# Kernel tuning notes

Measured on AMD Instinct MI355X. Metric: run time of the kernel, lower is better.

## Reference

```python
import jax, jax.numpy as jnp
import numpy as np

T, B, I, H, L = 512, 32, 1024, 1024, 2


def setup_inputs() -> dict:
    key = jax.random.key(0)
    ks = jax.random.split(key, 10)
    stdv = 1.0 / np.sqrt(H)
    u = lambda k, shape: jax.random.uniform(k, shape, jnp.float32, -stdv, stdv)
    return {
        "x": jax.random.normal(ks[0], (T, B, I), jnp.float32),
        "h0": jnp.zeros((L, B, H), jnp.float32),
        "c0": jnp.zeros((L, B, H), jnp.float32),
        "W0": u(ks[1], (4 * H, I)),
        "R0": u(ks[2], (4 * H, H)),
        "bi0": u(ks[3], (4 * H,)),
        "bh0": u(ks[4], (4 * H,)),
        "W1": u(ks[5], (4 * H, H)),
        "R1": u(ks[6], (4 * H, H)),
        "bi1": u(ks[7], (4 * H,)),
        "bh1": u(ks[8], (4 * H,)),
    }


def _run_layer(x, h_init, c_init, W, R, bi, bh):
    # Precompute input projection for all timesteps: [T, B, 4H]
    xg = jnp.einsum('tbi,gi->tbg', x, W) + bi

    def step(carry, xg_t):
        h, c = carry
        gates = jax.nn.sigmoid(xg_t + h @ R.T + bh)  # [B, 4H]
        i_g, o_g, z_g, f_g = jnp.split(gates, 4, axis=-1)
        c = c * f_g + z_g - i_g          # subtractive cell update
        h = jax.nn.sigmoid(c) - o_g      # subtractive output
        return (h, c), h

    (hT, cT), out = jax.lax.scan(step, (h_init, c_init), xg)
    return out, hT, cT


def reference(x, h0, c0, W0, R0, bi0, bh0, W1, R1, bi1, bh1):
    layers = [(W0, R0, bi0, bh0), (W1, R1, bi1, bh1)]
    out = x
    h_finals, c_finals = [], []
    for l, (W, R, bi, bh) in enumerate(layers):
        out, hT, cT = _run_layer(out, h0[l], c0[l], W, R, bi, bh)
        h_finals.append(hT)
        c_finals.append(cT)
    return out, (jnp.stack(h_finals), jnp.stack(c_finals))
```

## Files before the change

kernel.cpp:

```cpp
#include <hip/hip_runtime.h>

typedef unsigned short ushort_t;
typedef unsigned int uint_t;
typedef __bf16 bf16x8 __attribute__((ext_vector_type(8)));
typedef float f32x4 __attribute__((ext_vector_type(4)));

#define T_STEPS 512
#define NWG 256

union bfu { uint4 u; bf16x8 v; };

__device__ __forceinline__ float bf2f(ushort_t u) {
  union { unsigned u; float f; } v; v.u = ((unsigned)u) << 16; return v.f;
}
__device__ __forceinline__ ushort_t f2bf(float f) {
  union { float f; unsigned u; } v; v.f = f;
  unsigned r = (v.u + 0x7FFFu + ((v.u >> 16) & 1u)) >> 16;
  return (ushort_t)r;
}
__device__ __forceinline__ uint_t pack2(float a, float b) {
  return (uint_t)f2bf(a) | ((uint_t)f2bf(b) << 16);
}
__device__ __forceinline__ float sigf(float x) {
  return 1.0f / (1.0f + __expf(-x));
}

__global__ void __launch_bounds__(256) cvt_f32_bf16(
    const float* __restrict__ in, ushort_t* __restrict__ outp, int n4) {
  int i = blockIdx.x * 256 + threadIdx.x;
  const int stride = gridDim.x * 256;
  for (; i < n4; i += stride) {
    float4 v = ((const float4*)in)[i];
    ushort4 o;
    o.x = f2bf(v.x); o.y = f2bf(v.y); o.z = f2bf(v.z); o.w = f2bf(v.w);
    ((ushort4*)outp)[i] = o;
  }
}

__global__ void __launch_bounds__(256) init_h(
    const float* __restrict__ h0_all, ushort_t* __restrict__ hpp0,
    ushort_t* __restrict__ hpp1) {
  int i = blockIdx.x * 256 + threadIdx.x;
  int l = i >> 13, j = i & 8191;
  float4 v = ((const float4*)(h0_all + l * 32768))[j];
  ushort4 o;
  o.x = f2bf(v.x); o.y = f2bf(v.y); o.z = f2bf(v.z); o.w = f2bf(v.w);
  ((ushort4*)(l ? (hpp1 + 32768) : (hpp0 + 98304)))[j] = o;
}

__global__ void __launch_bounds__(256, 1) gemm_xg(
    const float* __restrict__ X, const ushort_t* __restrict__ Wm,
    const float* __restrict__ bi, ushort_t* __restrict__ outp) {
  __shared__ char smem[65536];
  const int tid = threadIdx.x;
  const int lane = tid & 63, w = tid >> 6;
  const int m0 = blockIdx.x * 128, n0 = blockIdx.y * 128;
  const int wr = w >> 1, wc = w & 1;
  const int lr = lane & 15, kg = lane >> 4;
  const int ar_ = tid & 127;
  const int abq = (tid >> 7) * 4;

  f32x4 acc[4][4] = {};
  float4 fa[8];

  auto stageA_issue = [&](int kt) {
    const float* src = X + (size_t)(m0 + ar_) * 1024 + kt * 64 + abq * 8;
#pragma unroll
    for (int i = 0; i < 4; ++i) {
      fa[2 * i] = *(const float4*)(src + i * 8);
      fa[2 * i + 1] = *(const float4*)(src + i * 8 + 4);
    }
  };
  auto stageA_write = [&](int p) {
    char* sA = smem + p * 32768;
#pragma unroll
    for (int i = 0; i < 4; ++i) {
      int blk = abq + i;
      uint4 o;
      o.x = pack2(fa[2 * i].x, fa[2 * i].y);
      o.y = pack2(fa[2 * i].z, fa[2 * i].w);
      o.z = pack2(fa[2 * i + 1].x, fa[2 * i + 1].y);
      o.w = pack2(fa[2 * i + 1].z, fa[2 * i + 1].w);
      *(uint4*)(sA + ar_ * 128 + ((blk ^ (ar_ & 7)) << 4)) = o;
    }
  };
  auto stageB = [&](int kt, int p) {
    const int ks = kt * 64;
    char* sB = smem + p * 32768 + 16384;
#pragma unroll
    for (int i = 0; i < 4; ++i) {
      int wi = w * 4 + i;
      int e = wi * 64 + lane;
      int row = e >> 3, pb = e & 7;
      int kb = pb ^ (row & 7);
      const ushort_t* gB = Wm + (size_t)(n0 + row) * 1024 + ks + kb * 8;
      __builtin_amdgcn_global_load_lds(
          (const __attribute__((address_space(1))) void*)gB,
          (__attribute__((address_space(3))) void*)(sB + wi * 1024), 16, 0, 0);
    }
  };

  stageA_issue(0);
  stageB(0, 0);
  stageA_write(0);
  __syncthreads();
#pragma unroll 1
  for (int kt = 0; kt < 16; ++kt) {
    const int p = kt & 1;
    if (kt < 15) { stageA_issue(kt + 1); stageB(kt + 1, p ^ 1); }
    const char* sA = smem + p * 32768;
    const char* sB = sA + 16384;
#pragma unroll
    for (int k2 = 0; k2 < 2; ++k2) {
      bf16x8 af[4], bf[4];
#pragma unroll
      for (int mt = 0; mt < 4; ++mt) {
        int ar = wr * 64 + mt * 16 + lr;
        int kb = k2 * 4 + kg;
        af[mt] = *(const bf16x8*)(sA + ar * 128 + ((kb ^ (ar & 7)) << 4));
      }
#pragma unroll
      for (int nt = 0; nt < 4; ++nt) {
        int br = wc * 64 + nt * 16 + lr;
        int kb = k2 * 4 + kg;
        bf[nt] = *(const bf16x8*)(sB + br * 128 + ((kb ^ (br & 7)) << 4));
      }
#pragma unroll
      for (int mt = 0; mt < 4; ++mt)
#pragma unroll
        for (int nt = 0; nt < 4; ++nt)
          acc[mt][nt] = __builtin_amdgcn_mfma_f32_16x16x32_bf16(
              af[mt], bf[nt], acc[mt][nt], 0, 0, 0);
    }
    if (kt < 15) stageA_write(p ^ 1);
    __syncthreads();
  }
#pragma unroll
  for (int nt = 0; nt < 4; ++nt) {
    int gc = n0 + wc * 64 + nt * 16 + lr;
    int pc = ((gc & 1023) >> 3) * 32 + (gc & 7) * 4 + (gc >> 10);
    float bv = bi[gc];
#pragma unroll
    for (int mt = 0; mt < 4; ++mt) {
#pragma unroll
      for (int r = 0; r < 4; ++r) {
        int gr = m0 + wr * 64 + mt * 16 + kg * 4 + r;
        outp[(size_t)gr * 4096 + pc] = f2bf(acc[mt][nt][r] + bv);
      }
    }
  }
}

#define GLD4(dst, addr)                                        \
  asm volatile("global_load_dwordx4 %0, %1, off sc0 sc1"      \
               : "=v"(dst) : "v"(addr))
#define WAITN(N)                                               \
  do {                                                         \
    asm volatile("s_waitcnt vmcnt(" #N ")" ::: "memory");      \
    __builtin_amdgcn_sched_barrier(0);                         \
  } while (0)

__global__ void __launch_bounds__(512, 1) fused_rec(
    const ushort_t* __restrict__ xg0p, const float* __restrict__ R0,
    const float* __restrict__ R1, const float* __restrict__ W1,
    const float* __restrict__ bh0, const float* __restrict__ bi1,
    const float* __restrict__ bh1, const float* __restrict__ c0_all,
    float* __restrict__ out_f, float* __restrict__ hfinb,
    float* __restrict__ cfinb, ushort_t* __restrict__ hpp0,
    ushort_t* __restrict__ hpp1, uint_t* __restrict__ flags0,
    uint_t* __restrict__ flags1) {
  extern __shared__ char smem[];
  char* hl = smem;
  float* gl = (float*)(smem + 131072);

  const int tid = threadIdx.x;
  const int wg = blockIdx.x;
  const int layer = wg >> 7;
  const int wgl = wg & 127;
  const int j0 = wgl * 8;
  const int lane = tid & 63, w = tid >> 6;
  const int n16 = (w & 1) << 4;
  const int kq = w >> 1;
  const int lr16 = lane & 15, kg = lane >> 4;
  const int b = (tid >> 3) & 31, jj = tid & 7;
  const int rx = lr16 & 7;

  uint_t* fown = layer ? flags1 : flags0;
  uint_t* foth = layer ? flags0 : flags1;

  const int c = n16 + lr16;
  const int r_w = ((c >> 3) << 10) + j0 + (c & 7);
  bf16x8 breg[16];
  if (layer == 0) {
#pragma unroll
    for (int i = 0; i < 8; ++i) {
      const float* src = R0 + (size_t)r_w * 1024 + kq * 256 + i * 32 + kg * 8;
      float4 f0 = *(const float4*)src;
      float4 f1 = *(const float4*)(src + 4);
      bfu o;
      o.u.x = pack2(f0.x, f0.y); o.u.y = pack2(f0.z, f0.w);
      o.u.z = pack2(f1.x, f1.y); o.u.w = pack2(f1.z, f1.w);
      breg[i] = o.v;
    }
  } else {
#pragma unroll
    for (int i = 0; i < 16; ++i) {
      int k = kq * 512 + i * 32 + kg * 8;
      const float* src = (k < 1024) ? (R1 + (size_t)r_w * 1024 + k)
                                    : (W1 + (size_t)r_w * 1024 + (k - 1024));
      float4 f0 = *(const float4*)src;
      float4 f1 = *(const float4*)(src + 4);
      bfu o;
      o.u.x = pack2(f0.x, f0.y); o.u.y = pack2(f0.z, f0.w);
      o.u.z = pack2(f1.x, f1.y); o.u.w = pack2(f1.z, f1.w);
      breg[i] = o.v;
    }
  }

  float bhv[4];
#pragma unroll
  for (int g = 0; g < 4; ++g) {
    int gi = g * 1024 + j0 + jj;
    bhv[g] = layer ? (bi1[gi] + bh1[gi]) : bh0[gi];
  }
  const int cidx = b * 1024 + j0 + jj;
  float c_st = c0_all[layer * 32768 + cidx];
  uint_t* hppd = (uint_t*)(layer ? hpp1 : hpp0);

  const char* xgbase = (const char*)xg0p +
      ((size_t)b * 4096 + (size_t)wgl * 32 + (size_t)jj * 4) * 2;
  uint2 xgu = {0, 0}, xgn = {0, 0};
  if (layer == 0)
    asm volatile("global_load_dwordx2 %0, %1, off" : "=v"(xgu) : "v"(xgbase));
  __syncthreads();

#pragma unroll 1
  for (int t = 0; t < T_STEPS; ++t) {
    {
      const int genOwn = t;
      const int genOth = layer ? (t + 1) : (t - 3);
      if (tid < 128) {
        while ((int)__hip_atomic_load(&fown[tid], __ATOMIC_RELAXED,
                                      __HIP_MEMORY_SCOPE_AGENT) < genOwn)
          __builtin_amdgcn_s_sleep(1);
      } else if (tid < 256) {
        while ((int)__hip_atomic_load(&foth[tid - 128], __ATOMIC_RELAXED,
                                      __HIP_MEMORY_SCOPE_AGENT) < genOth)
          __builtin_amdgcn_s_sleep(1);
      }
      __syncthreads();
      asm volatile("" ::: "memory");
    }

    uint4 hv[16];
    if (layer == 0) {
      if (t + 1 < T_STEPS)
        asm volatile("global_load_dwordx2 %0, %1, off"
                     : "=v"(xgn) : "v"(xgbase + (size_t)(t + 1) * 262144));
      const char* hsrc =
          (const char*)hpp0 + (((t + 3) & 3) << 16) + tid * 16;
#pragma unroll
      for (int l = 0; l < 8; ++l) GLD4(hv[l], hsrc + l * 8192);
      WAITN(0);
#pragma unroll
      for (int l = 0; l < 8; ++l) {
        int idx = l * 512 + tid;
        int row = idx >> 7, kb = idx & 127;
        *(uint4*)(hl + row * 2048 + ((kb ^ (row & 7)) << 4)) = hv[l];
      }
    } else {
      const char* h1src =
          (const char*)hpp1 + (((t + 1) & 1) << 16) + tid * 16;
      const char* h0src =
          (const char*)hpp0 + ((t & 3) << 16) + tid * 16;
#pragma unroll
      for (int l = 0; l < 8; ++l) GLD4(hv[l], h1src + l * 8192);
#pragma unroll
      for (int l = 0; l < 8; ++l) GLD4(hv[8 + l], h0src + l * 8192);
      WAITN(8);
#pragma unroll
      for (int l = 0; l < 8; ++l) {
        int idx = l * 512 + tid;
        int row = idx >> 7, kb = idx & 127;
        *(uint4*)(hl + row * 2048 + ((kb ^ (row & 7)) << 4)) = hv[l];
      }
      WAITN(0);
#pragma unroll
      for (int l = 0; l < 8; ++l) {
        int idx = l * 512 + tid;
        int row = idx >> 7, kb = idx & 127;
        *(uint4*)(hl + 65536 + row * 2048 + ((kb ^ (row & 7)) << 4)) =
            hv[8 + l];
      }
    }
    __syncthreads();

    f32x4 acc0 = {0.f, 0.f, 0.f, 0.f}, acc1 = {0.f, 0.f, 0.f, 0.f};
    if (layer == 0) {
      const char* a0 = hl + lr16 * 2048;
      const char* a1 = hl + (16 + lr16) * 2048;
#pragma unroll
      for (int i = 0; i < 8; ++i) {
        int kb = kq * 32 + i * 4 + kg;
        bf16x8 av0 = *(const bf16x8*)(a0 + ((kb ^ rx) << 4));
        bf16x8 av1 = *(const bf16x8*)(a1 + ((kb ^ rx) << 4));
        acc0 = __builtin_amdgcn_mfma_f32_16x16x32_bf16(av0, breg[i], acc0,
                                                       0, 0, 0);
        acc1 = __builtin_amdgcn_mfma_f32_16x16x32_bf16(av1, breg[i], acc1,
                                                       0, 0, 0);
      }
    } else {
      const char* buf = hl + ((kq >> 1) ? 65536 : 0);
      const char* a0 = buf + lr16 * 2048;
      const char* a1 = buf + (16 + lr16) * 2048;
#pragma unroll
      for (int i = 0; i < 16; ++i) {
        int kb = (kq & 1) * 64 + i * 4 + kg;
        bf16x8 av0 = *(const bf16x8*)(a0 + ((kb ^ rx) << 4));
        bf16x8 av1 = *(const bf16x8*)(a1 + ((kb ^ rx) << 4));
        acc0 = __builtin_amdgcn_mfma_f32_16x16x32_bf16(av0, breg[i], acc0,
                                                       0, 0, 0);
        acc1 = __builtin_amdgcn_mfma_f32_16x16x32_bf16(av1, breg[i], acc1,
                                                       0, 0, 0);
      }
    }
#pragma unroll
    for (int r = 0; r < 4; ++r) {
      gl[(kq * 32 + kg * 4 + r) * 33 + n16 + lr16] = acc0[r];
      gl[(kq * 32 + 16 + kg * 4 + r) * 33 + n16 + lr16] = acc1[r];
    }
    __syncthreads();

    if (tid < 256) {
      float pre[4];
#pragma unroll
      for (int g = 0; g < 4; ++g) {
        int col = g * 8 + jj;
        pre[g] = gl[(0 * 32 + b) * 33 + col] + gl[(1 * 32 + b) * 33 + col] +
                 gl[(2 * 32 + b) * 33 + col] + gl[(3 * 32 + b) * 33 + col] +
                 bhv[g];
      }
      if (layer == 0) {
        pre[0] += bf2f((ushort_t)(xgu.x & 0xffff));
        pre[1] += bf2f((ushort_t)(xgu.x >> 16));
        pre[2] += bf2f((ushort_t)(xgu.y & 0xffff));
        pre[3] += bf2f((ushort_t)(xgu.y >> 16));
      }
      float ig = sigf(pre[0]), og = sigf(pre[1]);
      float zg = sigf(pre[2]), fg = sigf(pre[3]);
      c_st = c_st * fg + zg - ig;
      float hv_ = sigf(c_st) - og;
      if (layer) out_f[(size_t)t * 32768 + cidx] = hv_;

      ushort_t hb = f2bf(hv_);
      int partner = __shfl_down((int)hb, 1, 64);
      if ((tid & 1) == 0) {
        uint_t packed =
            (uint_t)hb | (((uint_t)(unsigned short)partner) << 16);
        uint_t* dst = hppd +
            ((layer ? ((t & 1) << 14) : ((t & 3) << 14)) + (cidx >> 1));
        asm volatile("global_store_dword %0, %1, off sc0 sc1"
                     :: "v"(dst), "v"(packed) : "memory");
      }
      if (t == T_STEPS - 1) {
        hfinb[layer * 32768 + cidx] = hv_;
        cfinb[layer * 32768 + cidx] = c_st;
      }
    }

    asm volatile("s_waitcnt vmcnt(0)" ::: "memory");
    __syncthreads();
    if (tid == 0)
      __hip_atomic_store(&fown[wgl], (uint_t)(t + 1), __ATOMIC_RELAXED,
                         __HIP_MEMORY_SCOPE_AGENT);
    if (layer == 0) xgu = xgn;
  }
}

extern "C" void kernel_launch(void* const* d_in, const int* in_sizes, int n_in,
                              void* d_out, int out_size, void* d_ws,
                              size_t ws_size, hipStream_t stream) {
  (void)in_sizes; (void)n_in; (void)out_size; (void)ws_size;
  const float* x = (const float*)d_in[0];
  const float* h0 = (const float*)d_in[1];
  const float* c0 = (const float*)d_in[2];
  const float* W0 = (const float*)d_in[3];
  const float* R0 = (const float*)d_in[4];
  const float* bi0 = (const float*)d_in[5];
  const float* bh0 = (const float*)d_in[6];
  const float* W1 = (const float*)d_in[7];
  const float* R1 = (const float*)d_in[8];
  const float* bi1 = (const float*)d_in[9];
  const float* bh1 = (const float*)d_in[10];
  float* outp = (float*)d_out;

  char* ws = (char*)d_ws;
  ushort_t* Wbf0 = (ushort_t*)ws;
  ushort_t* xg0p = (ushort_t*)(ws + 8388608);
  ushort_t* hpp0 = (ushort_t*)(ws + 8388608 + 134217728);
  ushort_t* hpp1 = (ushort_t*)((char*)hpp0 + 262144);
  uint_t* flags0 = (uint_t*)((char*)hpp1 + 131072);
  uint_t* flags1 = flags0 + 128;

  const int REC_LDS = 131072 + 4 * 32 * 33 * 4;
  (void)hipFuncSetAttribute((const void*)fused_rec,
                            hipFuncAttributeMaxDynamicSharedMemorySize,
                            REC_LDS);
  (void)hipMemsetAsync(flags0, 0, 256 * sizeof(uint_t), stream);

  float* hfinb = outp + 16777216;
  float* cfinb = hfinb + 65536;

  cvt_f32_bf16<<<dim3(1024), dim3(256), 0, stream>>>(W0, Wbf0, 1048576);
  init_h<<<dim3(64), dim3(256), 0, stream>>>(h0, hpp0, hpp1);
  gemm_xg<<<dim3(128, 32), dim3(256), 0, stream>>>(x, Wbf0, bi0, xg0p);
  fused_rec<<<dim3(NWG), dim3(512), REC_LDS, stream>>>(
      xg0p, R0, R1, W1, bh0, bi1, bh1, c0, outp, hfinb, cfinb,
      hpp0, hpp1, flags0, flags1);
}
```

Baseline: 4.425 ms.

## Prefetch layer-0 h one step ahead in layer 1 and split its GEMM

Layer-1 workgroups now compute the input-projection half (W1 times layer-0 h) from an h0 tile loaded in the previous step. They run it while the recurrent h1 tile is still in flight, then do the R1 half once h1 arrives. This needs layer 1 to wait for layer 0 to be two steps ahead instead of one. The xg prefetch register is dropped in favour of issuing the next load at the end of the step, and the partial-sum LDS layout is changed to a padded row-of-132 layout. The aim is to hide global-load latency on the serial critical path, at the cost of tighter cross-layer coupling and more registers.

```diff
diff --git a/kernel.cpp b/kernel.cpp
--- a/kernel.cpp
+++ b/kernel.cpp
@@ -204,10 +204,8 @@
     }
   } else {
 #pragma unroll
-    for (int i = 0; i < 16; ++i) {
-      int k = kq * 512 + i * 32 + kg * 8;
-      const float* src = (k < 1024) ? (R1 + (size_t)r_w * 1024 + k)
-                                    : (W1 + (size_t)r_w * 1024 + (k - 1024));
+    for (int i = 0; i < 8; ++i) {
+      const float* src = R1 + (size_t)r_w * 1024 + kq * 256 + i * 32 + kg * 8;
       float4 f0 = *(const float4*)src;
       float4 f1 = *(const float4*)(src + 4);
       bfu o;
@@ -215,6 +213,16 @@
       o.u.z = pack2(f1.x, f1.y); o.u.w = pack2(f1.z, f1.w);
       breg[i] = o.v;
     }
+#pragma unroll
+    for (int i = 0; i < 8; ++i) {
+      const float* src = W1 + (size_t)r_w * 1024 + kq * 256 + i * 32 + kg * 8;
+      float4 f0 = *(const float4*)src;
+      float4 f1 = *(const float4*)(src + 4);
+      bfu o;
+      o.u.x = pack2(f0.x, f0.y); o.u.y = pack2(f0.z, f0.w);
+      o.u.z = pack2(f1.x, f1.y); o.u.w = pack2(f1.z, f1.w);
+      breg[8 + i] = o.v;
+    }
   }
 
   float bhv[4];
@@ -229,16 +237,18 @@
 
   const char* xgbase = (const char*)xg0p +
       ((size_t)b * 4096 + (size_t)wgl * 32 + (size_t)jj * 4) * 2;
-  uint2 xgu = {0, 0}, xgn = {0, 0};
-  if (layer == 0)
+  uint2 xgu = {0, 0};
+  if (layer == 0 && tid < 256)
     asm volatile("global_load_dwordx2 %0, %1, off" : "=v"(xgu) : "v"(xgbase));
+  uint4 hv0p[8];
   __syncthreads();
 
 #pragma unroll 1
   for (int t = 0; t < T_STEPS; ++t) {
     {
       const int genOwn = t;
-      const int genOth = layer ? (t + 1) : (t - 3);
+      const int genOth =
+          layer ? ((t + 2 > T_STEPS) ? T_STEPS : (t + 2)) : (t - 3);
       if (tid < 128) {
         while ((int)__hip_atomic_load(&fown[tid], __ATOMIC_RELAXED,
                                       __HIP_MEMORY_SCOPE_AGENT) < genOwn)
@@ -252,11 +262,9 @@
       asm volatile("" ::: "memory");
     }
 
-    uint4 hv[16];
+    f32x4 acc0 = {0.f, 0.f, 0.f, 0.f}, acc1 = {0.f, 0.f, 0.f, 0.f};
     if (layer == 0) {
-      if (t + 1 < T_STEPS)
-        asm volatile("global_load_dwordx2 %0, %1, off"
-                     : "=v"(xgn) : "v"(xgbase + (size_t)(t + 1) * 262144));
+      uint4 hv[8];
       const char* hsrc =
           (const char*)hpp0 + (((t + 3) & 3) << 16) + tid * 16;
 #pragma unroll
@@ -268,35 +276,7 @@
         int row = idx >> 7, kb = idx & 127;
         *(uint4*)(hl + row * 2048 + ((kb ^ (row & 7)) << 4)) = hv[l];
       }
-    } else {
-      const char* h1src =
-          (const char*)hpp1 + (((t + 1) & 1) << 16) + tid * 16;
-      const char* h0src =
-          (const char*)hpp0 + ((t & 3) << 16) + tid * 16;
-#pragma unroll
-      for (int l = 0; l < 8; ++l) GLD4(hv[l], h1src + l * 8192);
-#pragma unroll
-      for (int l = 0; l < 8; ++l) GLD4(hv[8 + l], h0src + l * 8192);
-      WAITN(8);
-#pragma unroll
-      for (int l = 0; l < 8; ++l) {
-        int idx = l * 512 + tid;
-        int row = idx >> 7, kb = idx & 127;
-        *(uint4*)(hl + row * 2048 + ((kb ^ (row & 7)) << 4)) = hv[l];
-      }
-      WAITN(0);
-#pragma unroll
-      for (int l = 0; l < 8; ++l) {
-        int idx = l * 512 + tid;
-        int row = idx >> 7, kb = idx & 127;
-        *(uint4*)(hl + 65536 + row * 2048 + ((kb ^ (row & 7)) << 4)) =
-            hv[8 + l];
-      }
-    }
-    __syncthreads();
-
-    f32x4 acc0 = {0.f, 0.f, 0.f, 0.f}, acc1 = {0.f, 0.f, 0.f, 0.f};
-    if (layer == 0) {
+      __syncthreads();
       const char* a0 = hl + lr16 * 2048;
       const char* a1 = hl + (16 + lr16) * 2048;
 #pragma unroll
@@ -310,24 +290,70 @@
                                                        0, 0, 0);
       }
     } else {
-      const char* buf = hl + ((kq >> 1) ? 65536 : 0);
-      const char* a0 = buf + lr16 * 2048;
-      const char* a1 = buf + (16 + lr16) * 2048;
-#pragma unroll
-      for (int i = 0; i < 16; ++i) {
-        int kb = (kq & 1) * 64 + i * 4 + kg;
-        bf16x8 av0 = *(const bf16x8*)(a0 + ((kb ^ rx) << 4));
-        bf16x8 av1 = *(const bf16x8*)(a1 + ((kb ^ rx) << 4));
-        acc0 = __builtin_amdgcn_mfma_f32_16x16x32_bf16(av0, breg[i], acc0,
-                                                       0, 0, 0);
-        acc1 = __builtin_amdgcn_mfma_f32_16x16x32_bf16(av1, breg[i], acc1,
-                                                       0, 0, 0);
+      if (t == 0) {
+        const char* h0src = (const char*)hpp0 + tid * 16;
+#pragma unroll
+        for (int l = 0; l < 8; ++l) GLD4(hv0p[l], h0src + l * 8192);
+      }
+      WAITN(0);
+#pragma unroll
+      for (int l = 0; l < 8; ++l) {
+        int idx = l * 512 + tid;
+        int row = idx >> 7, kb = idx & 127;
+        *(uint4*)(hl + 65536 + row * 2048 + ((kb ^ (row & 7)) << 4)) =
+            hv0p[l];
+      }
+      uint4 hv1[8];
+      const char* h1src =
+          (const char*)hpp1 + (((t + 1) & 1) << 16) + tid * 16;
+#pragma unroll
+      for (int l = 0; l < 8; ++l) GLD4(hv1[l], h1src + l * 8192);
+      const char* h0n =
+          (const char*)hpp0 + (((t + 1) & 3) << 16) + tid * 16;
+#pragma unroll
+      for (int l = 0; l < 8; ++l) GLD4(hv0p[l], h0n + l * 8192);
+      __syncthreads();
+      {
+        const char* a0 = hl + 65536 + lr16 * 2048;
+        const char* a1 = hl + 65536 + (16 + lr16) * 2048;
+#pragma unroll
+        for (int i = 0; i < 8; ++i) {
+          int kb = kq * 32 + i * 4 + kg;
+          bf16x8 av0 = *(const bf16x8*)(a0 + ((kb ^ rx) << 4));
+          bf16x8 av1 = *(const bf16x8*)(a1 + ((kb ^ rx) << 4));
+          acc0 = __builtin_amdgcn_mfma_f32_16x16x32_bf16(av0, breg[8 + i],
+                                                         acc0, 0, 0, 0);
+          acc1 = __builtin_amdgcn_mfma_f32_16x16x32_bf16(av1, breg[8 + i],
+                                                         acc1, 0, 0, 0);
+        }
+      }
+      WAITN(8);
+#pragma unroll
+      for (int l = 0; l < 8; ++l) {
+        int idx = l * 512 + tid;
+        int row = idx >> 7, kb = idx & 127;
+        *(uint4*)(hl + row * 2048 + ((kb ^ (row & 7)) << 4)) = hv1[l];
+      }
+      __syncthreads();
+      {
+        const char* a0 = hl + lr16 * 2048;
+        const char* a1 = hl + (16 + lr16) * 2048;
+#pragma unroll
+        for (int i = 0; i < 8; ++i) {
+          int kb = kq * 32 + i * 4 + kg;
+          bf16x8 av0 = *(const bf16x8*)(a0 + ((kb ^ rx) << 4));
+          bf16x8 av1 = *(const bf16x8*)(a1 + ((kb ^ rx) << 4));
+          acc0 = __builtin_amdgcn_mfma_f32_16x16x32_bf16(av0, breg[i], acc0,
+                                                         0, 0, 0);
+          acc1 = __builtin_amdgcn_mfma_f32_16x16x32_bf16(av1, breg[i], acc1,
+                                                         0, 0, 0);
+        }
       }
     }
 #pragma unroll
     for (int r = 0; r < 4; ++r) {
-      gl[(kq * 32 + kg * 4 + r) * 33 + n16 + lr16] = acc0[r];
-      gl[(kq * 32 + 16 + kg * 4 + r) * 33 + n16 + lr16] = acc1[r];
+      gl[(kg * 4 + r) * 132 + kq * 33 + n16 + lr16] = acc0[r];
+      gl[(16 + kg * 4 + r) * 132 + kq * 33 + n16 + lr16] = acc1[r];
     }
     __syncthreads();
 
@@ -336,8 +362,8 @@
 #pragma unroll
       for (int g = 0; g < 4; ++g) {
         int col = g * 8 + jj;
-        pre[g] = gl[(0 * 32 + b) * 33 + col] + gl[(1 * 32 + b) * 33 + col] +
-                 gl[(2 * 32 + b) * 33 + col] + gl[(3 * 32 + b) * 33 + col] +
+        pre[g] = gl[b * 132 + 0 * 33 + col] + gl[b * 132 + 1 * 33 + col] +
+                 gl[b * 132 + 2 * 33 + col] + gl[b * 132 + 3 * 33 + col] +
                  bhv[g];
       }
       if (layer == 0) {
@@ -373,7 +399,9 @@
     if (tid == 0)
       __hip_atomic_store(&fown[wgl], (uint_t)(t + 1), __ATOMIC_RELAXED,
                          __HIP_MEMORY_SCOPE_AGENT);
-    if (layer == 0) xgu = xgn;
+    if (layer == 0 && tid < 256 && t + 1 < T_STEPS)
+      asm volatile("global_load_dwordx2 %0, %1, off"
+                   : "=v"(xgu) : "v"(xgbase + (size_t)(t + 1) * 262144));
   }
 }
 
@@ -402,7 +430,7 @@
   uint_t* flags0 = (uint_t*)((char*)hpp1 + 131072);
   uint_t* flags1 = flags0 + 128;
 
-  const int REC_LDS = 131072 + 4 * 32 * 33 * 4;
+  const int REC_LDS = 131072 + 32 * 132 * 4;
   (void)hipFuncSetAttribute((const void*)fused_rec,
                             hipFuncAttributeMaxDynamicSharedMemorySize,
                             REC_LDS);
```

Measured after the change: 4.320 ms. -2.4%, faster.
